# Performance work log

Measured on AMD Instinct MI355X. Metric: run time of the kernel, lower is better.

Reference implementation:

```python
import jax, jax.numpy as jnp
import numpy as np


def binarize(t):
    # sign binarizer to exactly +/-1 (sign(0) -> +1), matching is_binary_tensor check
    return jnp.where(t >= 0, 1.0, -1.0).astype(t.dtype)


def setup_inputs() -> dict:
    key = jax.random.key(0)
    kx, kw, kb = jax.random.split(key, 3)
    x = jax.random.normal(kx, (32, 256, 56, 56), dtype=jnp.float32)
    weight = jax.random.normal(kw, (256, 256, 3, 3), dtype=jnp.float32)
    bias = jax.random.normal(kb, (256,), dtype=jnp.float32)
    return {"x": x, "weight": weight, "bias": bias}


def reference(x, weight, bias):
    bx = binarize(x)            # [B, Cin, H, W] in {-1, +1}
    bw = binarize(weight)       # [Cout, Cin, kh, kw] in {-1, +1}
    # F.conv2d(stride=1, padding=1, dilation=1, groups=1)
    out = jax.lax.conv_general_dilated(
        bx, bw,
        window_strides=(1, 1),
        padding=((1, 1), (1, 1)),
        dimension_numbers=("NCHW", "OIHW", "NCHW"),
    )
    return out + bias[None, :, None, None]
```

## Files before the change

### kernel.cpp

```cpp
#include <hip/hip_runtime.h>
#include <cstdint>

constexpr int B = 32, C = 256, H = 56, W = 56;
constexpr int HW = H * W;
constexpr int WORDS = C / 32;
constexpr int TAPS = 9;
constexpr int WPC = TAPS * WORDS;
constexpr int PH = H + 2, PW = W + 2, PHW = PH * PW;

__global__ __launch_bounds__(256) void pack_x_kernel(const float* __restrict__ x,
                                                     uint32_t* __restrict__ px) {
    int idx = blockIdx.x * 256 + threadIdx.x;
    int pp = idx % PHW;
    int r = idx / PHW;
    int wd = r % WORDS;
    int b = r / WORDS;
    int ph = pp / PW, pwp = pp - ph * PW;
    uint32_t bits = 0;
    if (ph >= 1 && ph <= H && pwp >= 1 && pwp <= W) {
        const float* xp = x + ((size_t)b * C + wd * 32) * HW + (size_t)(ph - 1) * W + (pwp - 1);
        #pragma unroll
        for (int i = 0; i < 32; ++i)
            bits |= (xp[(size_t)i * HW] < 0.0f ? (1u << i) : 0u);
    }
    px[((size_t)(b * PH + ph) * PW + pwp) * WORDS + wd] = bits;
}

__global__ __launch_bounds__(256) void pack_w_kernel(const float* __restrict__ wt,
                                                     uint32_t* __restrict__ pw) {
    int gid = blockIdx.x * 256 + threadIdx.x;
    int lane = gid & 63;
    int wv = gid >> 6;
    int pr = wv & 3;
    int ct = wv >> 2;
    int tap = ct % 9;
    int co = ct / 9;
    int ci = pr * 64 + lane;
    float v = wt[((size_t)co * C + ci) * TAPS + tap];
    unsigned long long m = __ballot(v < 0.0f);
    if (lane == 0) {
        pw[(size_t)co * WPC + tap * WORDS + pr * 2]     = (uint32_t)m;
        pw[(size_t)co * WPC + tap * WORDS + pr * 2 + 1] = (uint32_t)(m >> 32);
    }
}

__global__ __launch_bounds__(256) void basec_kernel(const uint32_t* __restrict__ pw,
                                                    const float* __restrict__ bias,
                                                    float* __restrict__ basec) {
    int idx = blockIdx.x * 256 + threadIdx.x;
    int co = idx & (C - 1);
    int cls = idx >> 8;
    int clsh = cls / 3, clsw = cls - clsh * 3;
    int nvalid = 0, invsum = 0;
    #pragma unroll
    for (int t = 0; t < TAPS; ++t) {
        int dh = t / 3 - 1, dw = t % 3 - 1;
        bool vh = !((dh == -1 && clsh == 0) || (dh == 1 && clsh == 2));
        bool vw = !((dw == -1 && clsw == 0) || (dw == 1 && clsw == 2));
        if (vh && vw) {
            ++nvalid;
        } else {
            int p = 0;
            #pragma unroll
            for (int k = 0; k < WORDS; ++k)
                p += __popc(pw[(size_t)co * WPC + t * WORDS + k]);
            invsum += p;
        }
    }
    basec[idx] = (float)(256 * nvalid + 2 * invsum) + bias[co];
}

__global__ __launch_bounds__(256) void bconv_kernel(const uint32_t* __restrict__ px,
                                                    const uint32_t* __restrict__ pw,
                                                    const float* __restrict__ basec,
                                                    float* __restrict__ out) {
    const int lane = threadIdx.x & 63;
    const int wid = __builtin_amdgcn_readfirstlane(threadIdx.x >> 6);
    const int hw = blockIdx.x * 64 + lane;
    const int b = blockIdx.y;
    const int h = hw / W;
    const int w = hw - h * W;

    uint32_t pxr[TAPS][WORDS];
    #pragma unroll
    for (int t = 0; t < TAPS; ++t) {
        const int dh = t / 3 - 1, dw = t - (t / 3) * 3 - 1;
        const uint4* p = reinterpret_cast<const uint4*>(
            px + ((size_t)(b * PH + (h + 1 + dh)) * PW + (w + 1 + dw)) * WORDS);
        uint4 a = p[0], q = p[1];
        pxr[t][0] = a.x; pxr[t][1] = a.y; pxr[t][2] = a.z; pxr[t][3] = a.w;
        pxr[t][4] = q.x; pxr[t][5] = q.y; pxr[t][6] = q.z; pxr[t][7] = q.w;
    }

    const int clsh = (h == 0) ? 0 : ((h == H - 1) ? 2 : 1);
    const int clsw = (w == 0) ? 0 : ((w == W - 1) ? 2 : 1);
    const int cobase = wid * 64;
    const float* bp = basec + (clsh * 3 + clsw) * C + cobase;
    const uint32_t* wbase = pw + (size_t)cobase * WPC;
    float* op = out + ((size_t)b * C + cobase) * HW + hw;

    #pragma unroll 1
    for (int j = 0; j < 64; ++j) {
        const uint32_t* wr = wbase + (size_t)j * WPC;
        uint32_t a0 = 0, a1 = 0, a2 = 0, a3 = 0;
        #pragma unroll
        for (int t = 0; t < TAPS; ++t) {
            a0 += __popc(pxr[t][0] ^ wr[t * WORDS + 0]);
            a1 += __popc(pxr[t][1] ^ wr[t * WORDS + 1]);
            a2 += __popc(pxr[t][2] ^ wr[t * WORDS + 2]);
            a3 += __popc(pxr[t][3] ^ wr[t * WORDS + 3]);
            a0 += __popc(pxr[t][4] ^ wr[t * WORDS + 4]);
            a1 += __popc(pxr[t][5] ^ wr[t * WORDS + 5]);
            a2 += __popc(pxr[t][6] ^ wr[t * WORDS + 6]);
            a3 += __popc(pxr[t][7] ^ wr[t * WORDS + 7]);
        }
        uint32_t total = (a0 + a1) + (a2 + a3);
        op[(size_t)j * HW] = fmaf(-2.0f, (float)(int)total, bp[j]);
    }
}

extern "C" void kernel_launch(void* const* d_in, const int* in_sizes, int n_in,
                              void* d_out, int out_size, void* d_ws, size_t ws_size,
                              hipStream_t stream) {
    const float* x = (const float*)d_in[0];
    const float* wt = (const float*)d_in[1];
    const float* bias = (const float*)d_in[2];
    float* out = (float*)d_out;

    uint32_t* px = (uint32_t*)d_ws;
    uint32_t* pw = px + (size_t)B * PHW * WORDS;
    float* basec = (float*)(pw + (size_t)C * WPC);

    pack_x_kernel<<<(B * WORDS * PHW) / 256, 256, 0, stream>>>(x, px);
    pack_w_kernel<<<(C * TAPS * 4 * 64) / 256, 256, 0, stream>>>(wt, pw);
    basec_kernel<<<(9 * C) / 256, 256, 0, stream>>>(pw, bias, basec);

    dim3 grid(HW / 64, B);
    bconv_kernel<<<grid, 256, 0, stream>>>(px, pw, basec, out);
}
```

Before: 387.3 us.

## Map threads to output channels with weights in registers and vectorize packing

```diff
diff --git a/kernel.cpp b/kernel.cpp
--- a/kernel.cpp
+++ b/kernel.cpp
@@ -3,27 +3,49 @@
 
 constexpr int B = 32, C = 256, H = 56, W = 56;
 constexpr int HW = H * W;
-constexpr int WORDS = C / 32;
+constexpr int WORDS = 8;
 constexpr int TAPS = 9;
 constexpr int WPC = TAPS * WORDS;
 constexpr int PH = H + 2, PW = W + 2, PHW = PH * PW;
 
+__global__ __launch_bounds__(256) void pad_zero_kernel(uint32_t* __restrict__ px) {
+    int idx = blockIdx.x * 256 + threadIdx.x;
+    int wd = idx & 7;
+    int r = idx >> 3;
+    int ring = r % 228;
+    int b = r / 228;
+    int ph, pwp;
+    if (ring < 58)       { ph = 0;              pwp = ring; }
+    else if (ring < 116) { ph = 57;             pwp = ring - 58; }
+    else if (ring < 172) { ph = 1 + (ring - 116); pwp = 0; }
+    else                 { ph = 1 + (ring - 172); pwp = 57; }
+    px[((size_t)(b * PH + ph) * PW + pwp) * WORDS + wd] = 0u;
+}
+
 __global__ __launch_bounds__(256) void pack_x_kernel(const float* __restrict__ x,
                                                      uint32_t* __restrict__ px) {
     int idx = blockIdx.x * 256 + threadIdx.x;
-    int pp = idx % PHW;
-    int r = idx / PHW;
-    int wd = r % WORDS;
-    int b = r / WORDS;
-    int ph = pp / PW, pwp = pp - ph * PW;
-    uint32_t bits = 0;
-    if (ph >= 1 && ph <= H && pwp >= 1 && pwp <= W) {
-        const float* xp = x + ((size_t)b * C + wd * 32) * HW + (size_t)(ph - 1) * W + (pwp - 1);
-        #pragma unroll
-        for (int i = 0; i < 32; ++i)
-            bits |= (xp[(size_t)i * HW] < 0.0f ? (1u << i) : 0u);
+    int hw4 = idx % 784;
+    int r = idx / 784;
+    int wd = r & 7;
+    int b = r >> 3;
+    const float4* xp = reinterpret_cast<const float4*>(x + ((size_t)b * C + wd * 32) * HW) + hw4;
+    uint32_t w0 = 0, w1 = 0, w2 = 0, w3 = 0;
+    #pragma unroll
+    for (int i = 0; i < 32; ++i) {
+        float4 v = xp[(size_t)i * (HW / 4)];
+        w0 |= (__float_as_uint(v.x) >> 31) << i;
+        w1 |= (__float_as_uint(v.y) >> 31) << i;
+        w2 |= (__float_as_uint(v.z) >> 31) << i;
+        w3 |= (__float_as_uint(v.w) >> 31) << i;
     }
-    px[((size_t)(b * PH + ph) * PW + pwp) * WORDS + wd] = bits;
+    int hw = hw4 * 4;
+    #pragma unroll
+    for (int q = 0; q < 4; ++q) {
+        int h = (hw + q) / W, w = (hw + q) - h * W;
+        uint32_t val = (q == 0) ? w0 : (q == 1) ? w1 : (q == 2) ? w2 : w3;
+        px[((size_t)(b * PH + h + 1) * PW + (w + 1)) * WORDS + wd] = val;
+    }
 }
 
 __global__ __launch_bounds__(256) void pack_w_kernel(const float* __restrict__ wt,
@@ -44,78 +66,84 @@
     }
 }
 
-__global__ __launch_bounds__(256) void basec_kernel(const uint32_t* __restrict__ pw,
+__global__ __launch_bounds__(256) void bconv_kernel(const uint32_t* __restrict__ px,
+                                                    const uint32_t* __restrict__ pw,
                                                     const float* __restrict__ bias,
-                                                    float* __restrict__ basec) {
-    int idx = blockIdx.x * 256 + threadIdx.x;
-    int co = idx & (C - 1);
-    int cls = idx >> 8;
-    int clsh = cls / 3, clsw = cls - clsh * 3;
-    int nvalid = 0, invsum = 0;
+                                                    float* __restrict__ out) {
+    const int lane = threadIdx.x & 63;
+    const int wid = threadIdx.x >> 6;
+    const int co = wid * 64 + lane;
+    const int hwbase = blockIdx.x * 64;
+    const int b = blockIdx.y;
+
+    uint32_t wreg[WPC];
+    {
+        const uint4* wp = reinterpret_cast<const uint4*>(pw + (size_t)co * WPC);
+        #pragma unroll
+        for (int i = 0; i < 18; ++i) {
+            uint4 v = wp[i];
+            wreg[i * 4 + 0] = v.x; wreg[i * 4 + 1] = v.y;
+            wreg[i * 4 + 2] = v.z; wreg[i * 4 + 3] = v.w;
+        }
+    }
+    uint32_t tp[TAPS];
     #pragma unroll
     for (int t = 0; t < TAPS; ++t) {
-        int dh = t / 3 - 1, dw = t % 3 - 1;
-        bool vh = !((dh == -1 && clsh == 0) || (dh == 1 && clsh == 2));
-        bool vw = !((dw == -1 && clsw == 0) || (dw == 1 && clsw == 2));
-        if (vh && vw) {
-            ++nvalid;
-        } else {
-            int p = 0;
-            #pragma unroll
-            for (int k = 0; k < WORDS; ++k)
-                p += __popc(pw[(size_t)co * WPC + t * WORDS + k]);
-            invsum += p;
-        }
-    }
-    basec[idx] = (float)(256 * nvalid + 2 * invsum) + bias[co];
-}
-
-__global__ __launch_bounds__(256) void bconv_kernel(const uint32_t* __restrict__ px,
-                                                    const uint32_t* __restrict__ pw,
-                                                    const float* __restrict__ basec,
-                                                    float* __restrict__ out) {
-    const int lane = threadIdx.x & 63;
-    const int wid = __builtin_amdgcn_readfirstlane(threadIdx.x >> 6);
-    const int hw = blockIdx.x * 64 + lane;
-    const int b = blockIdx.y;
-    const int h = hw / W;
-    const int w = hw - h * W;
-
-    uint32_t pxr[TAPS][WORDS];
-    #pragma unroll
-    for (int t = 0; t < TAPS; ++t) {
-        const int dh = t / 3 - 1, dw = t - (t / 3) * 3 - 1;
-        const uint4* p = reinterpret_cast<const uint4*>(
-            px + ((size_t)(b * PH + (h + 1 + dh)) * PW + (w + 1 + dw)) * WORDS);
-        uint4 a = p[0], q = p[1];
-        pxr[t][0] = a.x; pxr[t][1] = a.y; pxr[t][2] = a.z; pxr[t][3] = a.w;
-        pxr[t][4] = q.x; pxr[t][5] = q.y; pxr[t][6] = q.z; pxr[t][7] = q.w;
+        uint32_t s = 0;
+        #pragma unroll
+        for (int k = 0; k < WORDS; ++k) s += __popc(wreg[t * WORDS + k]);
+        tp[t] = s;
     }
 
-    const int clsh = (h == 0) ? 0 : ((h == H - 1) ? 2 : 1);
-    const int clsw = (w == 0) ? 0 : ((w == W - 1) ? 2 : 1);
-    const int cobase = wid * 64;
-    const float* bp = basec + (clsh * 3 + clsw) * C + cobase;
-    const uint32_t* wbase = pw + (size_t)cobase * WPC;
-    float* op = out + ((size_t)b * C + cobase) * HW + hw;
+    const float basep = 2304.0f + bias[co];
+    float* outrow = out + ((size_t)b * C + co) * HW + hwbase;
 
     #pragma unroll 1
-    for (int j = 0; j < 64; ++j) {
-        const uint32_t* wr = wbase + (size_t)j * WPC;
-        uint32_t a0 = 0, a1 = 0, a2 = 0, a3 = 0;
+    for (int p4 = 0; p4 < 16; ++p4) {
+        float o0, o1, o2, o3;
         #pragma unroll
-        for (int t = 0; t < TAPS; ++t) {
-            a0 += __popc(pxr[t][0] ^ wr[t * WORDS + 0]);
-            a1 += __popc(pxr[t][1] ^ wr[t * WORDS + 1]);
-            a2 += __popc(pxr[t][2] ^ wr[t * WORDS + 2]);
-            a3 += __popc(pxr[t][3] ^ wr[t * WORDS + 3]);
-            a0 += __popc(pxr[t][4] ^ wr[t * WORDS + 4]);
-            a1 += __popc(pxr[t][5] ^ wr[t * WORDS + 5]);
-            a2 += __popc(pxr[t][6] ^ wr[t * WORDS + 6]);
-            a3 += __popc(pxr[t][7] ^ wr[t * WORDS + 7]);
+        for (int q = 0; q < 4; ++q) {
+            const int p = p4 * 4 + q;
+            const int hw = hwbase + p;
+            const int h = hw / W;
+            const int w = hw - h * W;
+            const uint32_t* rp = px + ((size_t)(b * PH + h) * PW + w) * WORDS;
+            uint32_t a0 = 0, a1 = 0, a2 = 0, a3 = 0;
+            #pragma unroll
+            for (int row = 0; row < 3; ++row) {
+                const uint32_t* rr = rp + row * (PW * WORDS);
+                #pragma unroll
+                for (int c = 0; c < 3; ++c) {
+                    const int t = row * 3 + c;
+                    a0 += __popc(rr[c * 8 + 0] ^ wreg[t * 8 + 0]);
+                    a1 += __popc(rr[c * 8 + 1] ^ wreg[t * 8 + 1]);
+                    a2 += __popc(rr[c * 8 + 2] ^ wreg[t * 8 + 2]);
+                    a3 += __popc(rr[c * 8 + 3] ^ wreg[t * 8 + 3]);
+                    a0 += __popc(rr[c * 8 + 4] ^ wreg[t * 8 + 4]);
+                    a1 += __popc(rr[c * 8 + 5] ^ wreg[t * 8 + 5]);
+                    a2 += __popc(rr[c * 8 + 6] ^ wreg[t * 8 + 6]);
+                    a3 += __popc(rr[c * 8 + 7] ^ wreg[t * 8 + 7]);
+                }
+            }
+            const uint32_t total = (a0 + a1) + (a2 + a3);
+            float base2 = basep;
+            if (h == 0 || h == H - 1 || w == 0 || w == W - 1) {
+                uint32_t s = 0;
+                int ninv = 0;
+                #pragma unroll
+                for (int t = 0; t < TAPS; ++t) {
+                    const int dh = t / 3, dw = t % 3;
+                    const bool inv = (h == 0 && dh == 0) || (h == H - 1 && dh == 2) ||
+                                     (w == 0 && dw == 0) || (w == W - 1 && dw == 2);
+                    if (inv) { s += tp[t]; ++ninv; }
+                }
+                base2 = basep + (float)(2 * (int)s - 256 * ninv);
+            }
+            const float res = fmaf(-2.0f, (float)(int)total, base2);
+            if (q == 0) o0 = res; else if (q == 1) o1 = res;
+            else if (q == 2) o2 = res; else o3 = res;
         }
-        uint32_t total = (a0 + a1) + (a2 + a3);
-        op[(size_t)j * HW] = fmaf(-2.0f, (float)(int)total, bp[j]);
+        reinterpret_cast<float4*>(outrow)[p4] = make_float4(o0, o1, o2, o3);
     }
 }
 
@@ -129,12 +157,11 @@
 
     uint32_t* px = (uint32_t*)d_ws;
     uint32_t* pw = px + (size_t)B * PHW * WORDS;
-    float* basec = (float*)(pw + (size_t)C * WPC);
 
-    pack_x_kernel<<<(B * WORDS * PHW) / 256, 256, 0, stream>>>(x, px);
+    pad_zero_kernel<<<(B * 228 * WORDS) / 256, 256, 0, stream>>>(px);
+    pack_x_kernel<<<(B * WORDS * (HW / 4)) / 256, 256, 0, stream>>>(x, px);
     pack_w_kernel<<<(C * TAPS * 4 * 64) / 256, 256, 0, stream>>>(wt, pw);
-    basec_kernel<<<(9 * C) / 256, 256, 0, stream>>>(pw, bias, basec);
 
     dim3 grid(HW / 64, B);
-    bconv_kernel<<<grid, 256, 0, stream>>>(px, pw, basec, out);
+    bconv_kernel<<<grid, 256, 0, stream>>>(px, pw, bias, out);
 }
```

Measured after the change: 421.5 us. 8.8% more time.
